# Optimization experiments

Measured on AMD Instinct MI355X. Metric: run time of the kernel, lower is better.

The kernel has to match this reference:

```python
import jax, jax.numpy as jnp
import numpy as np

B, T, NE = 8, 4096, 1024
E, TOPK = 16, 2
LIN = NE + 32 + NE // 4 + NE // 4 + NE // 8 + NE // 8  # 1824
N_CITIES = 4


def setup_inputs() -> dict:
    key = jax.random.key(0)
    ks = jax.random.split(key, 11)
    s = 1.0 / np.sqrt(LIN)
    return {
        "mh_output": jax.random.normal(ks[0], (B, T, NE), jnp.float32),
        "delta_t_info": jax.random.normal(ks[1], (B, T, NE // 4), jnp.float32),
        "delta_dis_info": jax.random.normal(ks[2], (B, T, NE // 4), jnp.float32),
        "delta_rg_info": jax.random.normal(ks[3], (B, T, NE // 8), jnp.float32),
        "delta_entropy_info": jax.random.normal(ks[4], (B, T, NE // 8), jnp.float32),
        "city_embeddings": jax.random.normal(ks[5], (N_CITIES, 32), jnp.float32),
        "w_route": jax.random.uniform(ks[6], (LIN, E), jnp.float32, -s, s),
        "b_route": jax.random.uniform(ks[7], (E,), jnp.float32, -s, s),
        "w_noise": jax.random.uniform(ks[8], (LIN, E), jnp.float32, -s, s),
        "b_noise": jax.random.uniform(ks[9], (E,), jnp.float32, -s, s),
        "noise_eps": jax.random.normal(ks[10], (B, T, E), jnp.float32),
        "city_index": 0,
    }


def reference(mh_output, delta_t_info, delta_dis_info, delta_rg_info,
              delta_entropy_info, city_embeddings, w_route, b_route,
              w_noise, b_noise, noise_eps, city_index):
    b, t, _ = mh_output.shape
    city_embed = city_embeddings[city_index]  # [32]
    city_embeds = jnp.broadcast_to(city_embed[None, None, :], (b, t, 32))
    x = jnp.concatenate([mh_output, city_embeds, delta_t_info, delta_dis_info,
                         delta_rg_info, delta_entropy_info], axis=-1)  # [B,T,LIN]
    logits = jnp.einsum('btf,fe->bte', x, w_route) + b_route
    noise_logits = jnp.einsum('btf,fe->bte', x, w_noise) + b_noise
    noisy_logits = logits + noise_eps * jax.nn.softplus(noise_logits)  # training path
    gate1 = jax.nn.softmax(noisy_logits, axis=-1)
    top_k_logits, indices = jax.lax.top_k(noisy_logits, TOPK)  # [B,T,K]
    # scatter top-k values into a -inf tensor == mask non-topk entries to -inf
    mask = jnp.sum(jax.nn.one_hot(indices, noisy_logits.shape[-1], dtype=jnp.bool_), axis=-2) > 0
    sparse_logits = jnp.where(mask, noisy_logits, -jnp.inf)
    router_output = jax.nn.softmax(sparse_logits, axis=-1)
    return router_output, indices, gate1
```

## Files before the change

### kernel.cpp

```cpp
#include <hip/hip_runtime.h>
#include <math.h>


#define TOKS 64
#define NCHUNK 28
#define I_OFF 524288
#define G_OFF 589824
#define SS 36

__device__ __forceinline__ float softplus_f(float x) {
  return fmaxf(x, 0.0f) + log1pf(expf(-fabsf(x)));
}

__device__ __forceinline__ float get_comp(const float4& v, int kk) {
  return kk == 0 ? v.x : kk == 1 ? v.y : kk == 2 ? v.z : v.w;
}

__device__ __forceinline__ void dma16(const float* g, float* l) {
  __builtin_amdgcn_global_load_lds(
      (const __attribute__((address_space(1))) void*)g,
      (__attribute__((address_space(3))) void*)l, 16, 0, 0);
}

__global__ __launch_bounds__(512, 2) void router_kernel(
    const float* __restrict__ mh, const float* __restrict__ dt,
    const float* __restrict__ dd, const float* __restrict__ rg,
    const float* __restrict__ de, const float* __restrict__ cemb_all,
    const float* __restrict__ w_route, const float* __restrict__ b_route,
    const float* __restrict__ w_noise, const float* __restrict__ b_noise,
    const float* __restrict__ eps, const int* __restrict__ city_index,
    float* __restrict__ out) {
  __shared__ float smem[12288];
  float* sA0 = smem;
  float* sA1 = smem + 4096;
  float* sW0 = smem + 8192;
  float* sW1 = smem + 10240;
  float* sS  = smem;
  float* cityL = smem + 2304;

  const int tid = threadIdx.x;
  const int w   = tid >> 6;
  const int ln  = tid & 63;
  const int tg  = ln & 15;
  const int eg  = ln >> 4;
  const int blockTok = blockIdx.x * TOKS;

  float4 accL[4], accH[4];
#pragma unroll
  for (int j = 0; j < 4; ++j) {
    accL[j] = make_float4(0.f, 0.f, 0.f, 0.f);
    accH[j] = make_float4(0.f, 0.f, 0.f, 0.f);
  }

  auto a_src = [&](int g, int row) -> const float* {
    const float* base; int stride;
    if (g < 16)      { base = mh + g * 64;        stride = 1024; }
    else if (g < 20) { base = dt + (g - 16) * 64; stride = 256; }
    else if (g < 24) { base = dd + (g - 20) * 64; stride = 256; }
    else             { base = (g < 26) ? rg + (g - 24) * 64
                                       : de + (g - 26) * 64;
                       stride = 128; }
    return base + (size_t)(blockTok + row) * stride;
  };

  auto stageDMA = [&](int g, float* Abuf, float* Wbuf) {
#pragma unroll
    for (int i = 0; i < 2; ++i) {
      const int slot = i * 512 + tid;
      const int r    = slot >> 4;
      const int c4   = (slot & 15) ^ (r & 15);
      dma16(a_src(g, r) + c4 * 4, Abuf + slot * 4);
    }
    {
      const int r  = tid >> 3;
      const int c4 = tid & 7;
      const int kb = g * 64 + ((g >= 16) ? 32 : 0) + r;
      const float* ws = (c4 < 4) ? (w_route + kb * 16 + c4 * 4)
                                 : (w_noise + kb * 16 + (c4 - 4) * 4);
      dma16(ws, Wbuf + tid * 4);
    }
  };

  stageDMA(0, sA0, sW0);
  asm volatile("s_waitcnt vmcnt(0)" ::: "memory");
  __syncthreads();

  const int c4x0 = (((w << 1) | 0) ^ tg) << 2;
  const int c4x1 = (((w << 1) | 1) ^ tg) << 2;
  const int k0 = w * 8;

  for (int c = 0; c < NCHUNK; ++c) {
    const float* A = (c & 1) ? sA1 : sA0;
    const float* W = (c & 1) ? sW1 : sW0;

    if (c + 1 < NCHUNK)
      stageDMA(c + 1, (c & 1) ? sA0 : sA1, (c & 1) ? sW0 : sW1);

#pragma unroll
    for (int q = 0; q < 2; ++q) {
      const int cofs = q ? c4x1 : c4x0;
      float4 a[4];
#pragma unroll
      for (int j = 0; j < 4; ++j)
        a[j] = *(const float4*)&A[(tg + 16 * j) * 64 + cofs];
#pragma unroll
      for (int kk = 0; kk < 4; ++kk) {
        const int krow = k0 + q * 4 + kk;
        float4 wv0 = *(const float4*)&W[krow * 32 + eg * 8];
        float4 wv1 = *(const float4*)&W[krow * 32 + eg * 8 + 4];
#pragma unroll
        for (int j = 0; j < 4; ++j) {
          const float s = get_comp(a[j], kk);
          accL[j].x = fmaf(s, wv0.x, accL[j].x);
          accL[j].y = fmaf(s, wv0.y, accL[j].y);
          accL[j].z = fmaf(s, wv0.z, accL[j].z);
          accL[j].w = fmaf(s, wv0.w, accL[j].w);
          accH[j].x = fmaf(s, wv1.x, accH[j].x);
          accH[j].y = fmaf(s, wv1.y, accH[j].y);
          accH[j].z = fmaf(s, wv1.z, accH[j].z);
          accH[j].w = fmaf(s, wv1.w, accH[j].w);
        }
      }
    }

    asm volatile("s_waitcnt vmcnt(0)" ::: "memory");
    __syncthreads();
  }

  if (tid < 32) {
    const int e = tid & 15;
    const float* wsrc = (tid < 16) ? w_route : w_noise;
    const float* bsrc = (tid < 16) ? b_route : b_noise;
    const float* ce = cemb_all + city_index[0] * 32;
    float sacc = bsrc[e];
#pragma unroll
    for (int j = 0; j < 32; ++j)
      sacc = fmaf(ce[j], wsrc[(1024 + j) * 16 + e], sacc);
    cityL[tid] = sacc;
  }

  for (int r = 0; r < 8; ++r) {
    if (w == r) {
#pragma unroll
      for (int j = 0; j < 4; ++j) {
        float* p = &sS[(tg + 16 * j) * SS + eg * 8];
        if (r == 0) {
          *(float4*)(p)     = accL[j];
          *(float4*)(p + 4) = accH[j];
        } else {
          float4 x0 = *(float4*)(p), x1 = *(float4*)(p + 4);
          x0.x += accL[j].x; x0.y += accL[j].y; x0.z += accL[j].z; x0.w += accL[j].w;
          x1.x += accH[j].x; x1.y += accH[j].y; x1.z += accH[j].z; x1.w += accH[j].w;
          *(float4*)(p)     = x0;
          *(float4*)(p + 4) = x1;
        }
      }
    }
    __syncthreads();
  }

  if (tid < TOKS) {
    const int tokg = blockTok + tid;
    float l[32];
#pragma unroll
    for (int e4 = 0; e4 < 8; ++e4) {
      float4 s0 = *(const float4*)&sS[tid * SS + e4 * 4];
      l[e4 * 4 + 0] = s0.x; l[e4 * 4 + 1] = s0.y;
      l[e4 * 4 + 2] = s0.z; l[e4 * 4 + 3] = s0.w;
    }
#pragma unroll
    for (int e = 0; e < 32; ++e) l[e] += cityL[e];

    const float* ep = eps + (size_t)tokg * 16;
    float n[16];
#pragma unroll
    for (int e = 0; e < 16; ++e)
      n[e] = fmaf(ep[e], softplus_f(l[16 + e]), l[e]);

    float m1 = -INFINITY; int i1 = 0;
#pragma unroll
    for (int e = 0; e < 16; ++e)
      if (n[e] > m1) { m1 = n[e]; i1 = e; }
    float m2 = -INFINITY; int i2 = 0;
#pragma unroll
    for (int e = 0; e < 16; ++e)
      if (e != i1 && n[e] > m2) { m2 = n[e]; i2 = e; }

    float ex[16], Z = 0.f;
#pragma unroll
    for (int e = 0; e < 16; ++e) { ex[e] = expf(n[e] - m1); Z += ex[e]; }
    const float invZ  = 1.0f / Z;
    const float invZ2 = 1.0f / (1.0f + expf(m2 - m1));

    float r[16], g1[16];
#pragma unroll
    for (int e = 0; e < 16; ++e) {
      r[e]  = (e == i1 || e == i2) ? ex[e] * invZ2 : 0.0f;
      g1[e] = ex[e] * invZ;
    }

    float* ro = out + (size_t)tokg * 16;
#pragma unroll
    for (int e4 = 0; e4 < 4; ++e4)
      *(float4*)(ro + e4 * 4) = make_float4(r[e4*4], r[e4*4+1], r[e4*4+2], r[e4*4+3]);

    out[I_OFF + (size_t)tokg * 2 + 0] = (float)i1;
    out[I_OFF + (size_t)tokg * 2 + 1] = (float)i2;

    float* go = out + G_OFF + (size_t)tokg * 16;
#pragma unroll
    for (int e4 = 0; e4 < 4; ++e4)
      *(float4*)(go + e4 * 4) = make_float4(g1[e4*4], g1[e4*4+1], g1[e4*4+2], g1[e4*4+3]);
  }
}

extern "C" void kernel_launch(void* const* d_in, const int* in_sizes, int n_in,
                              void* d_out, int out_size, void* d_ws, size_t ws_size,
                              hipStream_t stream) {
  const float* mh = (const float*)d_in[0];
  const float* dt = (const float*)d_in[1];
  const float* dd = (const float*)d_in[2];
  const float* rg = (const float*)d_in[3];
  const float* de = (const float*)d_in[4];
  const float* ce = (const float*)d_in[5];
  const float* wr = (const float*)d_in[6];
  const float* br = (const float*)d_in[7];
  const float* wn = (const float*)d_in[8];
  const float* bn = (const float*)d_in[9];
  const float* ep = (const float*)d_in[10];
  const int*   ci = (const int*)d_in[11];
  float* out = (float*)d_out;

  router_kernel<<<512, 512, 0, stream>>>(mh, dt, dd, rg, de, ce, wr, br, wn, bn,
                                         ep, ci, out);
}
```

Before: 295.0 us.

## Split router GEMM over K into four slices with a separate epilogue kernel

The fused kernel becomes two kernels. A GEMM kernel splits the 28 K-chunks into four interleaved groups, each block handling 128 tokens and writing partial logits to workspace. A separate epilogue kernel sums the partials, adds the city and bias terms, and computes softplus noise, top-2 and both softmaxes. Each block now holds 128 tokens with a single-buffered weight tile staged through registers, which raises register pressure and adds workspace traffic plus a second launch in exchange for more parallelism.

```diff
diff --git a/kernel.cpp b/kernel.cpp
--- a/kernel.cpp
+++ b/kernel.cpp
@@ -2,8 +2,7 @@
 #include <math.h>
 
 
-#define TOKS 64
-#define NCHUNK 28
+#define NCHUNK 7
 #define I_OFF 524288
 #define G_OFF 589824
 #define SS 36
@@ -22,32 +21,27 @@
       (__attribute__((address_space(3))) void*)l, 16, 0, 0);
 }
 
-__global__ __launch_bounds__(512, 2) void router_kernel(
+__global__ __launch_bounds__(512, 2) void router_gemm(
     const float* __restrict__ mh, const float* __restrict__ dt,
     const float* __restrict__ dd, const float* __restrict__ rg,
-    const float* __restrict__ de, const float* __restrict__ cemb_all,
-    const float* __restrict__ w_route, const float* __restrict__ b_route,
-    const float* __restrict__ w_noise, const float* __restrict__ b_noise,
-    const float* __restrict__ eps, const int* __restrict__ city_index,
-    float* __restrict__ out) {
-  __shared__ float smem[12288];
-  float* sA0 = smem;
-  float* sA1 = smem + 4096;
-  float* sW0 = smem + 8192;
-  float* sW1 = smem + 10240;
-  float* sS  = smem;
-  float* cityL = smem + 2304;
+    const float* __restrict__ de, const float* __restrict__ w_route,
+    const float* __restrict__ w_noise, float* __restrict__ ws) {
+  __shared__ float smem[18432];
+  float* sW = smem + 16384;
+  float* sS = smem;
 
   const int tid = threadIdx.x;
   const int w   = tid >> 6;
   const int ln  = tid & 63;
   const int tg  = ln & 15;
   const int eg  = ln >> 4;
-  const int blockTok = blockIdx.x * TOKS;
-
-  float4 accL[4], accH[4];
-#pragma unroll
-  for (int j = 0; j < 4; ++j) {
+  const int tr  = blockIdx.x >> 2;
+  const int kg  = blockIdx.x & 3;
+  const int blockTok = tr * 128;
+
+  float4 accL[8], accH[8];
+#pragma unroll
+  for (int j = 0; j < 8; ++j) {
     accL[j] = make_float4(0.f, 0.f, 0.f, 0.f);
     accH[j] = make_float4(0.f, 0.f, 0.f, 0.f);
   }
@@ -63,70 +57,124 @@
     return base + (size_t)(blockTok + row) * stride;
   };
 
-  auto stageDMA = [&](int g, float* Abuf, float* Wbuf) {
-#pragma unroll
-    for (int i = 0; i < 2; ++i) {
+  auto stageA = [&](int g, float* Ab) {
+#pragma unroll
+    for (int i = 0; i < 4; ++i) {
       const int slot = i * 512 + tid;
       const int r    = slot >> 4;
       const int c4   = (slot & 15) ^ (r & 15);
-      dma16(a_src(g, r) + c4 * 4, Abuf + slot * 4);
-    }
-    {
-      const int r  = tid >> 3;
-      const int c4 = tid & 7;
-      const int kb = g * 64 + ((g >= 16) ? 32 : 0) + r;
-      const float* ws = (c4 < 4) ? (w_route + kb * 16 + c4 * 4)
-                                 : (w_noise + kb * 16 + (c4 - 4) * 4);
-      dma16(ws, Wbuf + tid * 4);
+      dma16(a_src(g, r) + c4 * 4, Ab + slot * 4);
     }
   };
-
-  stageDMA(0, sA0, sW0);
-  asm volatile("s_waitcnt vmcnt(0)" ::: "memory");
-  __syncthreads();
+  auto wglb = [&](int g) -> float4 {
+    const int r  = tid >> 3;
+    const int c4 = tid & 7;
+    const int kb = g * 64 + ((g >= 16) ? 32 : 0) + r;
+    const float* p = (c4 < 4) ? (w_route + kb * 16 + c4 * 4)
+                              : (w_noise + kb * 16 + (c4 - 4) * 4);
+    return *(const float4*)p;
+  };
+
+  float* A0 = smem;
+  float* A1 = smem + 8192;
+  float4 WRn;
+
+  {
+    const int g0 = kg;
+    WRn = wglb(g0);
+    stageA(g0, A0);
+    asm volatile("s_waitcnt vmcnt(0)" ::: "memory");
+    __syncthreads();
+    *(float4*)&sW[tid * 4] = WRn;
+    __syncthreads();
+  }
 
   const int c4x0 = (((w << 1) | 0) ^ tg) << 2;
   const int c4x1 = (((w << 1) | 1) ^ tg) << 2;
   const int k0 = w * 8;
 
-  for (int c = 0; c < NCHUNK; ++c) {
-    const float* A = (c & 1) ? sA1 : sA0;
-    const float* W = (c & 1) ? sW1 : sW0;
-
-    if (c + 1 < NCHUNK)
-      stageDMA(c + 1, (c & 1) ? sA0 : sA1, (c & 1) ? sW0 : sW1);
+  for (int j = 0; j < NCHUNK; ++j) {
+    const float* A = (j & 1) ? A1 : A0;
+
+    if (j + 1 < NCHUNK) {
+      stageA(kg + 4 * (j + 1), (j & 1) ? A0 : A1);
+      WRn = wglb(kg + 4 * (j + 1));
+    }
 
 #pragma unroll
     for (int q = 0; q < 2; ++q) {
       const int cofs = q ? c4x1 : c4x0;
-      float4 a[4];
-#pragma unroll
-      for (int j = 0; j < 4; ++j)
-        a[j] = *(const float4*)&A[(tg + 16 * j) * 64 + cofs];
+      float4 a[8];
+#pragma unroll
+      for (int jj = 0; jj < 8; ++jj)
+        a[jj] = *(const float4*)&A[(tg + 16 * jj) * 64 + cofs];
 #pragma unroll
       for (int kk = 0; kk < 4; ++kk) {
         const int krow = k0 + q * 4 + kk;
-        float4 wv0 = *(const float4*)&W[krow * 32 + eg * 8];
-        float4 wv1 = *(const float4*)&W[krow * 32 + eg * 8 + 4];
-#pragma unroll
-        for (int j = 0; j < 4; ++j) {
-          const float s = get_comp(a[j], kk);
-          accL[j].x = fmaf(s, wv0.x, accL[j].x);
-          accL[j].y = fmaf(s, wv0.y, accL[j].y);
-          accL[j].z = fmaf(s, wv0.z, accL[j].z);
-          accL[j].w = fmaf(s, wv0.w, accL[j].w);
-          accH[j].x = fmaf(s, wv1.x, accH[j].x);
-          accH[j].y = fmaf(s, wv1.y, accH[j].y);
-          accH[j].z = fmaf(s, wv1.z, accH[j].z);
-          accH[j].w = fmaf(s, wv1.w, accH[j].w);
+        float4 wv0 = *(const float4*)&sW[krow * 32 + eg * 8];
+        float4 wv1 = *(const float4*)&sW[krow * 32 + eg * 8 + 4];
+#pragma unroll
+        for (int jj = 0; jj < 8; ++jj) {
+          const float s = get_comp(a[jj], kk);
+          accL[jj].x = fmaf(s, wv0.x, accL[jj].x);
+          accL[jj].y = fmaf(s, wv0.y, accL[jj].y);
+          accL[jj].z = fmaf(s, wv0.z, accL[jj].z);
+          accL[jj].w = fmaf(s, wv0.w, accL[jj].w);
+          accH[jj].x = fmaf(s, wv1.x, accH[jj].x);
+          accH[jj].y = fmaf(s, wv1.y, accH[jj].y);
+          accH[jj].z = fmaf(s, wv1.z, accH[jj].z);
+          accH[jj].w = fmaf(s, wv1.w, accH[jj].w);
         }
       }
     }
 
-    asm volatile("s_waitcnt vmcnt(0)" ::: "memory");
+    if (j + 1 < NCHUNK) {
+      asm volatile("s_waitcnt vmcnt(0)" ::: "memory");
+      __syncthreads();
+      *(float4*)&sW[tid * 4] = WRn;
+      __syncthreads();
+    }
+  }
+  __syncthreads();
+
+  for (int r = 0; r < 8; ++r) {
+    if (w == r) {
+#pragma unroll
+      for (int jj = 0; jj < 8; ++jj) {
+        float* p = &sS[(tg + 16 * jj) * SS + eg * 8];
+        if (r == 0) {
+          *(float4*)(p)     = accL[jj];
+          *(float4*)(p + 4) = accH[jj];
+        } else {
+          float4 x0 = *(float4*)(p), x1 = *(float4*)(p + 4);
+          x0.x += accL[jj].x; x0.y += accL[jj].y; x0.z += accL[jj].z; x0.w += accL[jj].w;
+          x1.x += accH[jj].x; x1.y += accH[jj].y; x1.z += accH[jj].z; x1.w += accH[jj].w;
+          *(float4*)(p)     = x0;
+          *(float4*)(p + 4) = x1;
+        }
+      }
+    }
     __syncthreads();
   }
 
+  float* wsp = ws + (size_t)blockIdx.x * (128 * 32);
+#pragma unroll
+  for (int i = 0; i < 2; ++i) {
+    const int slot = i * 512 + tid;
+    const int tok  = slot >> 3;
+    const int e4   = slot & 7;
+    *(float4*)(wsp + slot * 4) = *(const float4*)&sS[tok * SS + e4 * 4];
+  }
+}
+
+__global__ __launch_bounds__(128) void router_epilogue(
+    const float* __restrict__ ws, const float* __restrict__ cemb_all,
+    const float* __restrict__ w_route, const float* __restrict__ b_route,
+    const float* __restrict__ w_noise, const float* __restrict__ b_noise,
+    const float* __restrict__ eps, const int* __restrict__ city_index,
+    float* __restrict__ out) {
+  __shared__ float city_l[32];
+  const int tid = threadIdx.x;
   if (tid < 32) {
     const int e = tid & 15;
     const float* wsrc = (tid < 16) ? w_route : w_noise;
@@ -136,82 +184,67 @@
 #pragma unroll
     for (int j = 0; j < 32; ++j)
       sacc = fmaf(ce[j], wsrc[(1024 + j) * 16 + e], sacc);
-    cityL[tid] = sacc;
-  }
-
-  for (int r = 0; r < 8; ++r) {
-    if (w == r) {
-#pragma unroll
-      for (int j = 0; j < 4; ++j) {
-        float* p = &sS[(tg + 16 * j) * SS + eg * 8];
-        if (r == 0) {
-          *(float4*)(p)     = accL[j];
-          *(float4*)(p + 4) = accH[j];
-        } else {
-          float4 x0 = *(float4*)(p), x1 = *(float4*)(p + 4);
-          x0.x += accL[j].x; x0.y += accL[j].y; x0.z += accL[j].z; x0.w += accL[j].w;
-          x1.x += accH[j].x; x1.y += accH[j].y; x1.z += accH[j].z; x1.w += accH[j].w;
-          *(float4*)(p)     = x0;
-          *(float4*)(p + 4) = x1;
-        }
-      }
-    }
-    __syncthreads();
-  }
-
-  if (tid < TOKS) {
-    const int tokg = blockTok + tid;
-    float l[32];
+    city_l[tid] = sacc;
+  }
+  __syncthreads();
+
+  const int t  = blockIdx.x * 128 + tid;
+  const int tr = t >> 7, tl = t & 127;
+
+  float l[32];
+#pragma unroll
+  for (int e = 0; e < 32; ++e) l[e] = city_l[e];
+#pragma unroll
+  for (int kg = 0; kg < 4; ++kg) {
+    const float* p = ws + (((size_t)(tr * 4 + kg) * 128) + tl) * 32;
 #pragma unroll
     for (int e4 = 0; e4 < 8; ++e4) {
-      float4 s0 = *(const float4*)&sS[tid * SS + e4 * 4];
-      l[e4 * 4 + 0] = s0.x; l[e4 * 4 + 1] = s0.y;
-      l[e4 * 4 + 2] = s0.z; l[e4 * 4 + 3] = s0.w;
-    }
-#pragma unroll
-    for (int e = 0; e < 32; ++e) l[e] += cityL[e];
-
-    const float* ep = eps + (size_t)tokg * 16;
-    float n[16];
-#pragma unroll
-    for (int e = 0; e < 16; ++e)
-      n[e] = fmaf(ep[e], softplus_f(l[16 + e]), l[e]);
-
-    float m1 = -INFINITY; int i1 = 0;
-#pragma unroll
-    for (int e = 0; e < 16; ++e)
-      if (n[e] > m1) { m1 = n[e]; i1 = e; }
-    float m2 = -INFINITY; int i2 = 0;
-#pragma unroll
-    for (int e = 0; e < 16; ++e)
-      if (e != i1 && n[e] > m2) { m2 = n[e]; i2 = e; }
-
-    float ex[16], Z = 0.f;
-#pragma unroll
-    for (int e = 0; e < 16; ++e) { ex[e] = expf(n[e] - m1); Z += ex[e]; }
-    const float invZ  = 1.0f / Z;
-    const float invZ2 = 1.0f / (1.0f + expf(m2 - m1));
-
-    float r[16], g1[16];
-#pragma unroll
-    for (int e = 0; e < 16; ++e) {
-      r[e]  = (e == i1 || e == i2) ? ex[e] * invZ2 : 0.0f;
-      g1[e] = ex[e] * invZ;
-    }
-
-    float* ro = out + (size_t)tokg * 16;
-#pragma unroll
-    for (int e4 = 0; e4 < 4; ++e4)
-      *(float4*)(ro + e4 * 4) = make_float4(r[e4*4], r[e4*4+1], r[e4*4+2], r[e4*4+3]);
-
-    out[I_OFF + (size_t)tokg * 2 + 0] = (float)i1;
-    out[I_OFF + (size_t)tokg * 2 + 1] = (float)i2;
-
-    float* go = out + G_OFF + (size_t)tokg * 16;
-#pragma unroll
-    for (int e4 = 0; e4 < 4; ++e4)
-      *(float4*)(go + e4 * 4) = make_float4(g1[e4*4], g1[e4*4+1], g1[e4*4+2], g1[e4*4+3]);
-  }
+      float4 v = *(const float4*)(p + e4 * 4);
+      l[e4 * 4 + 0] += v.x; l[e4 * 4 + 1] += v.y;
+      l[e4 * 4 + 2] += v.z; l[e4 * 4 + 3] += v.w;
+    }
+  }
+
+  const float* ep = eps + (size_t)t * 16;
+  float n[16];
+#pragma unroll
+  for (int e = 0; e < 16; ++e)
+    n[e] = fmaf(ep[e], softplus_f(l[16 + e]), l[e]);
+
+  float m1 = -INFINITY; int i1 = 0;
+#pragma unroll
+  for (int e = 0; e < 16; ++e)
+    if (n[e] > m1) { m1 = n[e]; i1 = e; }
+  float m2 = -INFINITY; int i2 = 0;
+#pragma unroll
+  for (int e = 0; e < 16; ++e)
+    if (e != i1 && n[e] > m2) { m2 = n[e]; i2 = e; }
+
+  float ex[16], Z = 0.f;
+#pragma unroll
+  for (int e = 0; e < 16; ++e) { ex[e] = expf(n[e] - m1); Z += ex[e]; }
+  const float invZ  = 1.0f / Z;
+  const float invZ2 = 1.0f / (1.0f + expf(m2 - m1));
+
+  float r[16], g1[16];
+#pragma unroll
+  for (int e = 0; e < 16; ++e) {
+    r[e]  = (e == i1 || e == i2) ? ex[e] * invZ2 : 0.0f;
+    g1[e] = ex[e] * invZ;
+  }
+
+  float* ro = out + (size_t)t * 16;
+#pragma unroll
+  for (int e4 = 0; e4 < 4; ++e4)
+    *(float4*)(ro + e4 * 4) = make_float4(r[e4*4], r[e4*4+1], r[e4*4+2], r[e4*4+3]);
+
+  out[I_OFF + (size_t)t * 2 + 0] = (float)i1;
+  out[I_OFF + (size_t)t * 2 + 1] = (float)i2;
+
+  float* go = out + G_OFF + (size_t)t * 16;
+#pragma unroll
+  for (int e4 = 0; e4 < 4; ++e4)
+    *(float4*)(go + e4 * 4) = make_float4(g1[e4*4], g1[e4*4+1], g1[e4*4+2], g1[e4*4+3]);
 }
 
 extern "C" void kernel_launch(void* const* d_in, const int* in_sizes, int n_in,
@@ -230,7 +263,8 @@
   const float* ep = (const float*)d_in[10];
   const int*   ci = (const int*)d_in[11];
   float* out = (float*)d_out;
-
-  router_kernel<<<512, 512, 0, stream>>>(mh, dt, dd, rg, de, ce, wr, br, wn, bn,
-                                         ep, ci, out);
-}
+  float* ws  = (float*)d_ws;
+
+  router_gemm<<<1024, 512, 0, stream>>>(mh, dt, dd, rg, de, wr, wn, ws);
+  router_epilogue<<<256, 128, 0, stream>>>(ws, ce, wr, br, wn, bn, ep, ci, out);
+}
```

Result: slower. 314.3 us (+6.6%).

## Enlarge router GEMM tile to 128 tokens by 128-K and stage weights via registers

Applied to the files above, without the earlier changes.

Each block now processes 128 tokens instead of 64, and each K-step covers 128 features instead of 64, so there are 14 steps instead of 28 and 256 blocks instead of 512. The A tile is still loaded with async global-to-LDS DMA into a double buffer. Weights are now prefetched into registers and written to a single LDS buffer after each step, and each thread holds twice as many accumulators. The aim is to halve per-step barrier overhead and reuse each weight load across more tokens. In exchange, LDS use rises to 144KB per block and register pressure grows, so occupancy drops to one block per CU and only 256 blocks are launched.

```diff
diff --git a/kernel.cpp b/kernel.cpp
--- a/kernel.cpp
+++ b/kernel.cpp
@@ -2,8 +2,7 @@
 #include <math.h>
 
 
-#define TOKS 64
-#define NCHUNK 28
+#define NSTEP 14
 #define I_OFF 524288
 #define G_OFF 589824
 #define SS 36
@@ -22,7 +21,7 @@
       (__attribute__((address_space(3))) void*)l, 16, 0, 0);
 }
 
-__global__ __launch_bounds__(512, 2) void router_kernel(
+__global__ __launch_bounds__(512, 1) void router_kernel(
     const float* __restrict__ mh, const float* __restrict__ dt,
     const float* __restrict__ dd, const float* __restrict__ rg,
     const float* __restrict__ de, const float* __restrict__ cemb_all,
@@ -30,101 +29,112 @@
     const float* __restrict__ w_noise, const float* __restrict__ b_noise,
     const float* __restrict__ eps, const int* __restrict__ city_index,
     float* __restrict__ out) {
-  __shared__ float smem[12288];
+  __shared__ float smem[36864];
   float* sA0 = smem;
-  float* sA1 = smem + 4096;
-  float* sW0 = smem + 8192;
-  float* sW1 = smem + 10240;
+  float* sA1 = smem + 16384;
+  float* sW  = smem + 32768;
   float* sS  = smem;
-  float* cityL = smem + 2304;
+  float* cityL = smem + 4608;
 
   const int tid = threadIdx.x;
   const int w   = tid >> 6;
   const int ln  = tid & 63;
   const int tg  = ln & 15;
   const int eg  = ln >> 4;
-  const int blockTok = blockIdx.x * TOKS;
-
-  float4 accL[4], accH[4];
-#pragma unroll
-  for (int j = 0; j < 4; ++j) {
+  const int blockTok = blockIdx.x * 128;
+
+  float4 accL[8], accH[8];
+#pragma unroll
+  for (int j = 0; j < 8; ++j) {
     accL[j] = make_float4(0.f, 0.f, 0.f, 0.f);
     accH[j] = make_float4(0.f, 0.f, 0.f, 0.f);
   }
 
-  auto a_src = [&](int g, int row) -> const float* {
-    const float* base; int stride;
-    if (g < 16)      { base = mh + g * 64;        stride = 1024; }
-    else if (g < 20) { base = dt + (g - 16) * 64; stride = 256; }
-    else if (g < 24) { base = dd + (g - 20) * 64; stride = 256; }
-    else             { base = (g < 26) ? rg + (g - 24) * 64
-                                       : de + (g - 26) * 64;
-                       stride = 128; }
-    return base + (size_t)(blockTok + row) * stride;
+  auto a_src = [&](int s, int r) -> const float* {
+    const size_t gr = blockTok + r;
+    if (s < 8)  return mh + gr * 1024 + s * 128;
+    if (s < 10) return dt + gr * 256 + (s - 8) * 128;
+    if (s < 12) return dd + gr * 256 + (s - 10) * 128;
+    if (s == 12) return rg + gr * 128;
+    return de + gr * 128;
   };
 
-  auto stageDMA = [&](int g, float* Abuf, float* Wbuf) {
+  auto stageA = [&](int s, float* Ab) {
+#pragma unroll
+    for (int i = 0; i < 8; ++i) {
+      const int slot = i * 512 + tid;
+      const int r    = slot >> 5;
+      const int p    = slot & 31;
+      const int c4   = (p & 16) | ((p & 15) ^ (r & 15));
+      dma16(a_src(s, r) + c4 * 4, Ab + slot * 4);
+    }
+  };
+
+  auto wglb = [&](int s, float4& w0, float4& w1) {
 #pragma unroll
     for (int i = 0; i < 2; ++i) {
       const int slot = i * 512 + tid;
-      const int r    = slot >> 4;
-      const int c4   = (slot & 15) ^ (r & 15);
-      dma16(a_src(g, r) + c4 * 4, Abuf + slot * 4);
-    }
-    {
-      const int r  = tid >> 3;
-      const int c4 = tid & 7;
-      const int kb = g * 64 + ((g >= 16) ? 32 : 0) + r;
-      const float* ws = (c4 < 4) ? (w_route + kb * 16 + c4 * 4)
-                                 : (w_noise + kb * 16 + (c4 - 4) * 4);
-      dma16(ws, Wbuf + tid * 4);
+      const int kr   = slot >> 3;
+      const int c4   = slot & 7;
+      const int wrow = s * 128 + ((s >= 8) ? 32 : 0) + kr;
+      const float* p = (c4 < 4) ? (w_route + wrow * 16 + c4 * 4)
+                                : (w_noise + wrow * 16 + (c4 - 4) * 4);
+      if (i == 0) w0 = *(const float4*)p; else w1 = *(const float4*)p;
     }
   };
 
-  stageDMA(0, sA0, sW0);
+  float4 WR0, WR1;
+  stageA(0, sA0);
+  wglb(0, WR0, WR1);
   asm volatile("s_waitcnt vmcnt(0)" ::: "memory");
   __syncthreads();
-
-  const int c4x0 = (((w << 1) | 0) ^ tg) << 2;
-  const int c4x1 = (((w << 1) | 1) ^ tg) << 2;
-  const int k0 = w * 8;
-
-  for (int c = 0; c < NCHUNK; ++c) {
-    const float* A = (c & 1) ? sA1 : sA0;
-    const float* W = (c & 1) ? sW1 : sW0;
-
-    if (c + 1 < NCHUNK)
-      stageDMA(c + 1, (c & 1) ? sA0 : sA1, (c & 1) ? sW0 : sW1);
-
-#pragma unroll
-    for (int q = 0; q < 2; ++q) {
-      const int cofs = q ? c4x1 : c4x0;
-      float4 a[4];
-#pragma unroll
-      for (int j = 0; j < 4; ++j)
-        a[j] = *(const float4*)&A[(tg + 16 * j) * 64 + cofs];
+  *(float4*)&sW[tid * 4]         = WR0;
+  *(float4*)&sW[(tid + 512) * 4] = WR1;
+  __syncthreads();
+
+  for (int s = 0; s < NSTEP; ++s) {
+    const float* A = (s & 1) ? sA1 : sA0;
+
+    if (s + 1 < NSTEP) {
+      stageA(s + 1, (s & 1) ? sA0 : sA1);
+      wglb(s + 1, WR0, WR1);
+    }
+
+#pragma unroll
+    for (int q = 0; q < 4; ++q) {
+      const int L  = w * 4 + q;
+      const int p4 = ((L & 16) | ((L & 15) ^ tg)) * 4;
+      float4 a[8];
+#pragma unroll
+      for (int j = 0; j < 8; ++j)
+        a[j] = *(const float4*)&A[(tg + 16 * j) * 128 + p4];
 #pragma unroll
       for (int kk = 0; kk < 4; ++kk) {
-        const int krow = k0 + q * 4 + kk;
-        float4 wv0 = *(const float4*)&W[krow * 32 + eg * 8];
-        float4 wv1 = *(const float4*)&W[krow * 32 + eg * 8 + 4];
-#pragma unroll
-        for (int j = 0; j < 4; ++j) {
-          const float s = get_comp(a[j], kk);
-          accL[j].x = fmaf(s, wv0.x, accL[j].x);
-          accL[j].y = fmaf(s, wv0.y, accL[j].y);
-          accL[j].z = fmaf(s, wv0.z, accL[j].z);
-          accL[j].w = fmaf(s, wv0.w, accL[j].w);
-          accH[j].x = fmaf(s, wv1.x, accH[j].x);
-          accH[j].y = fmaf(s, wv1.y, accH[j].y);
-          accH[j].z = fmaf(s, wv1.z, accH[j].z);
-          accH[j].w = fmaf(s, wv1.w, accH[j].w);
+        const int krow = L * 4 + kk;
+        float4 wv0 = *(const float4*)&sW[krow * 32 + eg * 8];
+        float4 wv1 = *(const float4*)&sW[krow * 32 + eg * 8 + 4];
+#pragma unroll
+        for (int j = 0; j < 8; ++j) {
+          const float sv = get_comp(a[j], kk);
+          accL[j].x = fmaf(sv, wv0.x, accL[j].x);
+          accL[j].y = fmaf(sv, wv0.y, accL[j].y);
+          accL[j].z = fmaf(sv, wv0.z, accL[j].z);
+          accL[j].w = fmaf(sv, wv0.w, accL[j].w);
+          accH[j].x = fmaf(sv, wv1.x, accH[j].x);
+          accH[j].y = fmaf(sv, wv1.y, accH[j].y);
+          accH[j].z = fmaf(sv, wv1.z, accH[j].z);
+          accH[j].w = fmaf(sv, wv1.w, accH[j].w);
         }
       }
     }
 
     asm volatile("s_waitcnt vmcnt(0)" ::: "memory");
     __syncthreads();
+    if (s + 1 < NSTEP) {
+      *(float4*)&sW[tid * 4]         = WR0;
+      *(float4*)&sW[(tid + 512) * 4] = WR1;
+      __syncthreads();
+    }
   }
 
   if (tid < 32) {
@@ -142,7 +152,7 @@
   for (int r = 0; r < 8; ++r) {
     if (w == r) {
 #pragma unroll
-      for (int j = 0; j < 4; ++j) {
+      for (int j = 0; j < 8; ++j) {
         float* p = &sS[(tg + 16 * j) * SS + eg * 8];
         if (r == 0) {
           *(float4*)(p)     = accL[j];
@@ -159,7 +169,7 @@
     __syncthreads();
   }
 
-  if (tid < TOKS) {
+  if (tid < 128) {
     const int tokg = blockTok + tid;
     float l[32];
 #pragma unroll
@@ -231,6 +241,6 @@
   const int*   ci = (const int*)d_in[11];
   float* out = (float*)d_out;
 
-  router_kernel<<<512, 512, 0, stream>>>(mh, dt, dd, rg, de, ce, wr, br, wn, bn,
+  router_kernel<<<256, 512, 0, stream>>>(mh, dt, dd, rg, de, ce, wr, br, wn, bn,
                                          ep, ci, out);
 }
```

New measurement: 343.9 us. 16.6% more time.

## Tree-reduce wave partial sums and hoist city bias and eps loads

Applied to the files above, without the earlier changes.

The 8-step serialized cross-wave reduction through shared memory becomes a 3-level tree reduction using separate smem slots. This cuts the number of barrier-separated steps and lets several waves work at once. The city-embedding bias is now computed during the first DMA wait into a dedicated shared array, and eps is loaded as float4 vectors before the reduction so that load latency overlaps. The costs are a little extra shared memory and more registers held live across the reduction.

```diff
diff --git a/kernel.cpp b/kernel.cpp
--- a/kernel.cpp
+++ b/kernel.cpp
@@ -6,7 +6,7 @@
 #define NCHUNK 28
 #define I_OFF 524288
 #define G_OFF 589824
-#define SS 36
+#define SP 36
 
 __device__ __forceinline__ float softplus_f(float x) {
   return fmaxf(x, 0.0f) + log1pf(expf(-fabsf(x)));
@@ -31,12 +31,11 @@
     const float* __restrict__ eps, const int* __restrict__ city_index,
     float* __restrict__ out) {
   __shared__ float smem[12288];
+  __shared__ float city_s[32];
   float* sA0 = smem;
   float* sA1 = smem + 4096;
   float* sW0 = smem + 8192;
   float* sW1 = smem + 10240;
-  float* sS  = smem;
-  float* cityL = smem + 2304;
 
   const int tid = threadIdx.x;
   const int w   = tid >> 6;
@@ -82,6 +81,19 @@
   };
 
   stageDMA(0, sA0, sW0);
+
+  if (tid < 32) {
+    const int e = tid & 15;
+    const float* wsrc = (tid < 16) ? w_route : w_noise;
+    const float* bsrc = (tid < 16) ? b_route : b_noise;
+    const float* ce = cemb_all + city_index[0] * 32;
+    float sacc = bsrc[e];
+#pragma unroll
+    for (int j = 0; j < 32; ++j)
+      sacc = fmaf(ce[j], wsrc[(1024 + j) * 16 + e], sacc);
+    city_s[tid] = sacc;
+  }
+
   asm volatile("s_waitcnt vmcnt(0)" ::: "memory");
   __syncthreads();
 
@@ -127,55 +139,73 @@
     __syncthreads();
   }
 
-  if (tid < 32) {
-    const int e = tid & 15;
-    const float* wsrc = (tid < 16) ? w_route : w_noise;
-    const float* bsrc = (tid < 16) ? b_route : b_noise;
-    const float* ce = cemb_all + city_index[0] * 32;
-    float sacc = bsrc[e];
-#pragma unroll
-    for (int j = 0; j < 32; ++j)
-      sacc = fmaf(ce[j], wsrc[(1024 + j) * 16 + e], sacc);
-    cityL[tid] = sacc;
-  }
-
-  for (int r = 0; r < 8; ++r) {
-    if (w == r) {
-#pragma unroll
-      for (int j = 0; j < 4; ++j) {
-        float* p = &sS[(tg + 16 * j) * SS + eg * 8];
-        if (r == 0) {
-          *(float4*)(p)     = accL[j];
-          *(float4*)(p + 4) = accH[j];
-        } else {
-          float4 x0 = *(float4*)(p), x1 = *(float4*)(p + 4);
-          x0.x += accL[j].x; x0.y += accL[j].y; x0.z += accL[j].z; x0.w += accL[j].w;
-          x1.x += accH[j].x; x1.y += accH[j].y; x1.z += accH[j].z; x1.w += accH[j].w;
-          *(float4*)(p)     = x0;
-          *(float4*)(p + 4) = x1;
-        }
-      }
-    }
-    __syncthreads();
+  float4 ep0, ep1, ep2, ep3;
+  if (tid < TOKS) {
+    const float* ep = eps + (size_t)(blockTok + tid) * 16;
+    ep0 = *(const float4*)(ep +  0);
+    ep1 = *(const float4*)(ep +  4);
+    ep2 = *(const float4*)(ep +  8);
+    ep3 = *(const float4*)(ep + 12);
+  }
+
+  auto writeP = [&](int slot) {
+    float* Sb = smem + slot * 2304;
+#pragma unroll
+    for (int j = 0; j < 4; ++j) {
+      float* p = &Sb[(tg + 16 * j) * SP + eg * 8];
+      *(float4*)(p)     = accL[j];
+      *(float4*)(p + 4) = accH[j];
+    }
+  };
+  auto addP = [&](int slot) {
+    const float* Sb = smem + slot * 2304;
+#pragma unroll
+    for (int j = 0; j < 4; ++j) {
+      const float* p = &Sb[(tg + 16 * j) * SP + eg * 8];
+      float4 x0 = *(const float4*)(p), x1 = *(const float4*)(p + 4);
+      accL[j].x += x0.x; accL[j].y += x0.y; accL[j].z += x0.z; accL[j].w += x0.w;
+      accH[j].x += x1.x; accH[j].y += x1.y; accH[j].z += x1.z; accH[j].w += x1.w;
+    }
+  };
+
+  if (w >= 4) writeP(w - 4);
+  __syncthreads();
+  if (w < 4) addP(w);
+  __syncthreads();
+  if (w == 2 || w == 3) writeP(w - 2);
+  __syncthreads();
+  if (w < 2) addP(w);
+  __syncthreads();
+  if (w == 1) writeP(0);
+  __syncthreads();
+  if (w == 0) {
+    addP(0);
+    writeP(0);
   }
 
   if (tid < TOKS) {
     const int tokg = blockTok + tid;
+    const float* Sb = smem + tid * SP;
     float l[32];
 #pragma unroll
     for (int e4 = 0; e4 < 8; ++e4) {
-      float4 s0 = *(const float4*)&sS[tid * SS + e4 * 4];
+      float4 s0 = *(const float4*)&Sb[e4 * 4];
       l[e4 * 4 + 0] = s0.x; l[e4 * 4 + 1] = s0.y;
       l[e4 * 4 + 2] = s0.z; l[e4 * 4 + 3] = s0.w;
     }
 #pragma unroll
-    for (int e = 0; e < 32; ++e) l[e] += cityL[e];
-
-    const float* ep = eps + (size_t)tokg * 16;
+    for (int e = 0; e < 32; ++e) l[e] += city_s[e];
+
     float n[16];
-#pragma unroll
-    for (int e = 0; e < 16; ++e)
-      n[e] = fmaf(ep[e], softplus_f(l[16 + e]), l[e]);
+    {
+      const float epv[16] = {ep0.x, ep0.y, ep0.z, ep0.w,
+                             ep1.x, ep1.y, ep1.z, ep1.w,
+                             ep2.x, ep2.y, ep2.z, ep2.w,
+                             ep3.x, ep3.y, ep3.z, ep3.w};
+#pragma unroll
+      for (int e = 0; e < 16; ++e)
+        n[e] = fmaf(epv[e], softplus_f(l[16 + e]), l[e]);
+    }
 
     float m1 = -INFINITY; int i1 = 0;
 #pragma unroll
```

Result: no change. 296.4 us (+0.5%).
